# Optimization experiments

Hardware: AMD Instinct MI355X
Metric: run time of the kernel (lower is better)

## Reference

```python
import jax, jax.numpy as jnp
import numpy as np

N_NODES = 50000
N_EDGES = 800000
N_REL = 4
F_IN = 128
H1 = 64          # RGCN out
HEADS = 4
D_H = 32         # per-head GAT out
N_GRAPHS = 64


def setup_inputs() -> dict:
    key = jax.random.key(0)
    ks = jax.random.split(key, 16)
    inp = {
        "x": jax.random.normal(ks[0], (N_NODES, F_IN), dtype=jnp.float32),
        "edge_index": jax.random.randint(ks[1], (2, N_EDGES), 0, N_NODES, dtype=jnp.int32),
        "edge_type": jax.random.randint(ks[2], (N_EDGES,), 0, N_REL, dtype=jnp.int32),
        "batch": jnp.sort(jax.random.randint(ks[3], (N_NODES,), 0, N_GRAPHS, dtype=jnp.int32)),
        # RGCNConv params (relation weights, root weight, bias)
        "W_rel": jax.random.normal(ks[4], (N_REL, F_IN, H1), dtype=jnp.float32) * 0.05,
        "W_root": jax.random.normal(ks[5], (F_IN, H1), dtype=jnp.float32) * 0.05,
        "b_rgcn": jnp.zeros((H1,), dtype=jnp.float32),
        # GATConv params
        "W_gat": jax.random.normal(ks[6], (H1, HEADS * D_H), dtype=jnp.float32) * 0.1,
        "att_src": jax.random.normal(ks[7], (HEADS, D_H), dtype=jnp.float32) * 0.1,
        "att_dst": jax.random.normal(ks[8], (HEADS, D_H), dtype=jnp.float32) * 0.1,
        "b_gat": jnp.zeros((HEADS * D_H,), dtype=jnp.float32),
        # dense layers
        "W1": jax.random.normal(ks[9], (HEADS * D_H, 16), dtype=jnp.float32) * 0.05,
        "b1": jnp.zeros((16,), dtype=jnp.float32),
        "W2": jax.random.normal(ks[10], (16, 1), dtype=jnp.float32) * 0.2,
        "b2": jnp.zeros((1,), dtype=jnp.float32),
    }
    return inp


def reference(x, W_rel, W_root, b_rgcn, W_gat, att_src, att_dst, b_gat,
              W1, b1, W2, b2, edge_index, edge_type, batch):
    src, dst = edge_index[0], edge_index[1]
    n = x.shape[0]

    # ---- RGCNConv: mean aggregation per relation, then linear (linearity lets
    # us aggregate raw features first, then apply W_rel) + root transform ----
    xs = x[src]                                            # [E, F_IN]
    out = x @ W_root + b_rgcn                              # [N, H1]
    for r in range(N_REL):
        mask = (edge_type == r).astype(x.dtype)            # [E]
        s = jax.ops.segment_sum(xs * mask[:, None], dst, num_segments=n)
        cnt = jax.ops.segment_sum(mask, dst, num_segments=n)
        mean_r = s / jnp.maximum(cnt, 1.0)[:, None]        # [N, F_IN]
        out = out + mean_r @ W_rel[r]
    h = jax.nn.relu(out)                                   # [N, H1]
    # (dropout omitted: deterministic/eval reference)

    # ---- GATConv (heads=4, concat, no self loops, edge_attr unused) ----
    g = (h @ W_gat).reshape(n, HEADS, D_H)                 # [N, H, D]
    a_s = jnp.einsum('nhd,hd->nh', g, att_src)             # [N, H]
    a_d = jnp.einsum('nhd,hd->nh', g, att_dst)
    e = jax.nn.leaky_relu(a_s[src] + a_d[dst], 0.2)        # [E, H]
    m = jax.ops.segment_max(e, dst, num_segments=n)        # [N, H]
    ex = jnp.exp(e - m[dst])                               # [E, H]
    den = jax.ops.segment_sum(ex, dst, num_segments=n)     # [N, H]
    alpha = ex / den[dst]
    o = jax.ops.segment_sum(alpha[:, :, None] * g[src], dst, num_segments=n)
    o = o.reshape(n, HEADS * D_H) + b_gat                  # [N, 128]
    o = jax.nn.leaky_relu(o, 0.01)

    # ---- dense1 -> leaky_relu -> global max pool -> dense2 ----
    z = jax.nn.leaky_relu(o @ W1 + b1, 0.01)               # [N, 16]
    p = jax.ops.segment_max(z, batch, num_segments=N_GRAPHS)  # [G, 16]
    y = p @ W2 + b2                                        # [G, 1]
    return y
```

## Files before the change

kernel.cpp:

```cpp
#include <hip/hip_runtime.h>
#include <hip/hip_bf16.h>

constexpr int N_NODES = 50000;
constexpr int N_EDGES = 800000;
constexpr int F_IN = 128;
constexpr int H1 = 64;
constexpr int HEADS = 4;
constexpr int D_H = 32;
constexpr int HOUT = HEADS * D_H;
constexpr int N_REL = 4;
constexpr int N_GRAPHS = 64;
constexpr int MBIG = H1 * (1 + N_REL);
constexpr int NBLK = (N_NODES + 255) / 256;

typedef __attribute__((ext_vector_type(8))) short bf16x8;
typedef __attribute__((ext_vector_type(4))) float f32x4;

__device__ __forceinline__ unsigned f2mono(float f) {
  unsigned u = __float_as_uint(f);
  return (u & 0x80000000u) ? ~u : (u | 0x80000000u);
}
__device__ __forceinline__ float mono2f(unsigned m) {
  unsigned u = (m & 0x80000000u) ? (m & 0x7FFFFFFFu) : ~m;
  return __uint_as_float(u);
}
constexpr unsigned MONO_NEG_INF = 0x007FFFFFu;

__device__ __forceinline__ unsigned short f2bf(float f) {
  unsigned u = __float_as_uint(f);
  unsigned r = (u + 0x7FFFu + ((u >> 16) & 1u)) >> 16;
  return (unsigned short)r;
}
__device__ __forceinline__ float bf2f(unsigned short h) {
  return __uint_as_float((unsigned)h << 16);
}
__device__ __forceinline__ float bflo(unsigned u) { return __uint_as_float(u << 16); }
__device__ __forceinline__ float bfhi(unsigned u) { return __uint_as_float(u & 0xFFFF0000u); }

__global__ __launch_bounds__(256) void build_wT(const float* __restrict__ W_root,
                                                const float* __restrict__ W_rel,
                                                const float* __restrict__ W_gat,
                                                unsigned short* __restrict__ WbT_hi,
                                                unsigned short* __restrict__ WbT_lo,
                                                unsigned short* __restrict__ WgT_hi,
                                                unsigned short* __restrict__ WgT_lo) {
  int i = blockIdx.x * 256 + threadIdx.x;
  if (i < MBIG * F_IN) {
    int c = i / F_IN, k = i % F_IN;
    float w = (c < H1) ? W_root[k * H1 + c]
                       : W_rel[((size_t)(((c - H1) >> 6) * F_IN + k)) * H1 + ((c - H1) & 63)];
    unsigned short hi = f2bf(w);
    WbT_hi[i] = hi;
    WbT_lo[i] = f2bf(w - bf2f(hi));
  } else {
    int j = i - MBIG * F_IN;
    if (j < HOUT * H1) {
      int c = j / H1, k = j % H1;
      float w = W_gat[k * HOUT + c];
      unsigned short hi = f2bf(w);
      WgT_hi[j] = hi;
      WgT_lo[j] = f2bf(w - bf2f(hi));
    }
  }
}

template <int K>
__global__ __launch_bounds__(256) void gemm_mfma(const float* __restrict__ A,
                                                 const unsigned short* __restrict__ BT_hi,
                                                 const unsigned short* __restrict__ BT_lo,
                                                 float* __restrict__ C,
                                                 unsigned short* __restrict__ Cbf,
                                                 int N, int M) {
  constexpr int Kp = K + 8;
  __shared__ unsigned short Ahi[64 * Kp];
  __shared__ unsigned short Alo[64 * Kp];
  const int tid = threadIdx.x;
  const int rowBase = blockIdx.x * 64;
  const int colBase = blockIdx.y * 64;
  constexpr int KQ = K >> 2;
  constexpr int slots = 64 * KQ;
  for (int s = tid; s < slots; s += 256) {
    int r = s / KQ, c4 = (s % KQ) * 4;
    int gr = rowBase + r;
    float4 v = make_float4(0.f, 0.f, 0.f, 0.f);
    if (gr < N) v = *reinterpret_cast<const float4*>(&A[(size_t)gr * K + c4]);
    ushort4 hi, lo;
    hi.x = f2bf(v.x); lo.x = f2bf(v.x - bf2f(hi.x));
    hi.y = f2bf(v.y); lo.y = f2bf(v.y - bf2f(hi.y));
    hi.z = f2bf(v.z); lo.z = f2bf(v.z - bf2f(hi.z));
    hi.w = f2bf(v.w); lo.w = f2bf(v.w - bf2f(hi.w));
    *reinterpret_cast<ushort4*>(&Ahi[r * Kp + c4]) = hi;
    *reinterpret_cast<ushort4*>(&Alo[r * Kp + c4]) = lo;
  }
  __syncthreads();
  const int wv = tid >> 6, lane = tid & 63;
  const int wr = (wv >> 1) * 32, wc = (wv & 1) * 32;
  const int lrow = lane & 15, lkc = lane >> 4;
  f32x4 acc[2][2] = {};
#pragma unroll
  for (int ks = 0; ks < K; ks += 32) {
    bf16x8 ah[2], al[2], bh[2], bl[2];
#pragma unroll
    for (int fr = 0; fr < 2; ++fr) {
      int r = wr + fr * 16 + lrow;
      ah[fr] = *reinterpret_cast<const bf16x8*>(&Ahi[r * Kp + ks + lkc * 8]);
      al[fr] = *reinterpret_cast<const bf16x8*>(&Alo[r * Kp + ks + lkc * 8]);
    }
#pragma unroll
    for (int fc = 0; fc < 2; ++fc) {
      int c = colBase + wc + fc * 16 + lrow;
      bh[fc] = *reinterpret_cast<const bf16x8*>(&BT_hi[(size_t)c * K + ks + lkc * 8]);
      bl[fc] = *reinterpret_cast<const bf16x8*>(&BT_lo[(size_t)c * K + ks + lkc * 8]);
    }
#pragma unroll
    for (int fr = 0; fr < 2; ++fr)
#pragma unroll
      for (int fc = 0; fc < 2; ++fc) {
        acc[fr][fc] = __builtin_amdgcn_mfma_f32_16x16x32_bf16(ah[fr], bh[fc], acc[fr][fc], 0, 0, 0);
        acc[fr][fc] = __builtin_amdgcn_mfma_f32_16x16x32_bf16(ah[fr], bl[fc], acc[fr][fc], 0, 0, 0);
        acc[fr][fc] = __builtin_amdgcn_mfma_f32_16x16x32_bf16(al[fr], bh[fc], acc[fr][fc], 0, 0, 0);
      }
  }
#pragma unroll
  for (int fr = 0; fr < 2; ++fr) {
#pragma unroll
    for (int i = 0; i < 4; ++i) {
      int row = rowBase + wr + fr * 16 + lkc * 4 + i;
      if (row < N) {
#pragma unroll
        for (int fc = 0; fc < 2; ++fc) {
          int col = colBase + wc + fc * 16 + lrow;
          float v = acc[fr][fc][i];
          if (C) C[(size_t)row * M + col] = v;
          if (Cbf) Cbf[(size_t)row * M + col] = f2bf(v);
        }
      }
    }
  }
}

__global__ __launch_bounds__(256) void k_hist(const int* __restrict__ dst,
                                              int* __restrict__ deg,
                                              int* __restrict__ rank) {
  int e = blockIdx.x * 256 + threadIdx.x;
  if (e < N_EDGES) rank[e] = atomicAdd(&deg[dst[e]], 1);
}

__global__ __launch_bounds__(256) void k_s1(const int* __restrict__ deg,
                                            int* __restrict__ bsum) {
  __shared__ int ss[256];
  int t = threadIdx.x;
  int i = blockIdx.x * 256 + t;
  ss[t] = (i < N_NODES) ? deg[i] : 0;
  __syncthreads();
  for (int d = 128; d > 0; d >>= 1) {
    if (t < d) ss[t] += ss[t + d];
    __syncthreads();
  }
  if (t == 0) bsum[blockIdx.x] = ss[0];
}

__global__ __launch_bounds__(256) void k_s2(const int* __restrict__ bsum,
                                            int* __restrict__ bbase,
                                            int* __restrict__ off) {
  __shared__ int ss[256];
  int t = threadIdx.x;
  int v = (t < NBLK) ? bsum[t] : 0;
  ss[t] = v;
  __syncthreads();
  for (int d = 1; d < 256; d <<= 1) {
    int u = (t >= d) ? ss[t - d] : 0;
    __syncthreads();
    ss[t] += u;
    __syncthreads();
  }
  if (t < NBLK) bbase[t] = ss[t] - v;
  if (t == NBLK - 1) off[N_NODES] = ss[t];
}

__global__ __launch_bounds__(256) void k_s3(const int* __restrict__ deg,
                                            const int* __restrict__ bbase,
                                            int* __restrict__ off) {
  __shared__ int ss[256];
  int t = threadIdx.x;
  int i = blockIdx.x * 256 + t;
  int v = (i < N_NODES) ? deg[i] : 0;
  ss[t] = v;
  __syncthreads();
  for (int d = 1; d < 256; d <<= 1) {
    int u = (t >= d) ? ss[t - d] : 0;
    __syncthreads();
    ss[t] += u;
    __syncthreads();
  }
  if (i < N_NODES) off[i] = bbase[blockIdx.x] + ss[t] - v;
}

__global__ __launch_bounds__(256) void k_fill(const int* __restrict__ src,
                                              const int* __restrict__ dst,
                                              const int* __restrict__ etype,
                                              const int* __restrict__ off,
                                              const int* __restrict__ rank,
                                              int* __restrict__ eprep) {
  int e = blockIdx.x * 256 + threadIdx.x;
  if (e >= N_EDGES) return;
  int pos = off[dst[e]] + rank[e];
  eprep[pos] = src[e] | (etype[e] << 16);
}

__global__ __launch_bounds__(256) void rgcn_gather(const unsigned short* __restrict__ xtbf,
                                                   const int* __restrict__ off,
                                                   const int* __restrict__ eprep,
                                                   const float* __restrict__ b_rgcn,
                                                   float* __restrict__ h) {
  int wid = (blockIdx.x * 256 + threadIdx.x) >> 6;
  int lane = threadIdx.x & 63;
  int half = lane >> 5;
  int cp = lane & 31;
  int start = off[wid], end = off[wid + 1];
  float a0x=0.f,a0y=0.f,a1x=0.f,a1y=0.f,a2x=0.f,a2y=0.f,a3x=0.f,a3y=0.f;
  int c0=0,c1=0,c2=0,c3=0;
  int niter = (end - start + 1) >> 1;
  for (int t = 0; t < niter; t += 2) {
    int idx0 = start + 2 * t + half;
    int idx1 = idx0 + 2;
    int p0 = (idx0 < end) ? eprep[idx0] : 0x70000;
    int p1 = (idx1 < end) ? eprep[idx1] : 0x70000;
    int s0 = p0 & 0xFFFF, r0 = p0 >> 16;
    int s1 = p1 & 0xFFFF, r1 = p1 >> 16;
    unsigned u0 = *reinterpret_cast<const unsigned*>(
        &xtbf[(size_t)s0 * MBIG + H1 + (r0 << 6) + cp * 2]);
    unsigned u1 = *reinterpret_cast<const unsigned*>(
        &xtbf[(size_t)s1 * MBIG + H1 + (r1 << 6) + cp * 2]);
    float v0x = bflo(u0), v0y = bfhi(u0);
    float v1x = bflo(u1), v1y = bfhi(u1);
    a0x += (r0==0)?v0x:0.f; a0y += (r0==0)?v0y:0.f; c0 += (r0==0);
    a1x += (r0==1)?v0x:0.f; a1y += (r0==1)?v0y:0.f; c1 += (r0==1);
    a2x += (r0==2)?v0x:0.f; a2y += (r0==2)?v0y:0.f; c2 += (r0==2);
    a3x += (r0==3)?v0x:0.f; a3y += (r0==3)?v0y:0.f; c3 += (r0==3);
    a0x += (r1==0)?v1x:0.f; a0y += (r1==0)?v1y:0.f; c0 += (r1==0);
    a1x += (r1==1)?v1x:0.f; a1y += (r1==1)?v1y:0.f; c1 += (r1==1);
    a2x += (r1==2)?v1x:0.f; a2y += (r1==2)?v1y:0.f; c2 += (r1==2);
    a3x += (r1==3)?v1x:0.f; a3y += (r1==3)?v1y:0.f; c3 += (r1==3);
  }
  a0x += __shfl_xor(a0x, 32); a0y += __shfl_xor(a0y, 32);
  a1x += __shfl_xor(a1x, 32); a1y += __shfl_xor(a1y, 32);
  a2x += __shfl_xor(a2x, 32); a2y += __shfl_xor(a2y, 32);
  a3x += __shfl_xor(a3x, 32); a3y += __shfl_xor(a3y, 32);
  c0 += __shfl_xor(c0, 32); c1 += __shfl_xor(c1, 32);
  c2 += __shfl_xor(c2, 32); c3 += __shfl_xor(c3, 32);
  if (half == 0) {
    unsigned ur = *reinterpret_cast<const unsigned*>(&xtbf[(size_t)wid * MBIG + cp * 2]);
    float2 bb = *reinterpret_cast<const float2*>(&b_rgcn[cp * 2]);
    float i0 = 1.0f / (float)max(c0, 1);
    float i1 = 1.0f / (float)max(c1, 1);
    float i2 = 1.0f / (float)max(c2, 1);
    float i3 = 1.0f / (float)max(c3, 1);
    float vx = bflo(ur) + bb.x + a0x * i0 + a1x * i1 + a2x * i2 + a3x * i3;
    float vy = bfhi(ur) + bb.y + a0y * i0 + a1y * i1 + a2y * i2 + a3y * i3;
    *reinterpret_cast<float2*>(&h[(size_t)wid * H1 + cp * 2]) =
        make_float2(fmaxf(vx, 0.f), fmaxf(vy, 0.f));
  }
}

__global__ __launch_bounds__(256) void gat_att(const unsigned short* __restrict__ gbf,
                                               const float* __restrict__ att_src,
                                               const float* __restrict__ att_dst,
                                               float* __restrict__ a_s,
                                               float* __restrict__ a_d) {
  __shared__ float gs[64][129];
  __shared__ float asrc[HOUT], adst[HOUT];
  int t = threadIdx.x;
  if (t < HOUT) { asrc[t] = att_src[t]; adst[t] = att_dst[t]; }
  int nb = blockIdx.x * 64;
#pragma unroll
  for (int it = 0; it < 8; ++it) {
    int idx = it * 256 + t;
    int r = idx >> 5, c4 = (idx & 31) * 4;
    int gn = nb + r;
    uint2 v = make_uint2(0u, 0u);
    if (gn < N_NODES)
      v = *reinterpret_cast<const uint2*>(&gbf[(size_t)gn * HOUT + c4]);
    gs[r][c4 + 0] = bflo(v.x); gs[r][c4 + 1] = bfhi(v.x);
    gs[r][c4 + 2] = bflo(v.y); gs[r][c4 + 3] = bfhi(v.y);
  }
  __syncthreads();
  int n = t & 63, hh = t >> 6;
  float s = 0.f, d = 0.f;
#pragma unroll
  for (int k = 0; k < D_H; ++k) {
    float gv = gs[n][hh * D_H + k];
    s += gv * asrc[hh * D_H + k];
    d += gv * adst[hh * D_H + k];
  }
  if (nb + n < N_NODES) {
    a_s[(size_t)(nb + n) * 4 + hh] = s;
    a_d[(size_t)(nb + n) * 4 + hh] = d;
  }
}

__global__ __launch_bounds__(256) void init_mono(unsigned* __restrict__ p, int count) {
  int i = blockIdx.x * 256 + threadIdx.x;
  if (i < count) p[i] = MONO_NEG_INF;
}

constexpr int GAT_BLOCKS = 2048;
constexpr int GAT_WAVES = GAT_BLOCKS * 4;
__global__ __launch_bounds__(256) void gat_fused(const unsigned short* __restrict__ gbf,
                                                 const float* __restrict__ a_s,
                                                 const float* __restrict__ a_d,
                                                 const int* __restrict__ off,
                                                 const int* __restrict__ eprep,
                                                 const float* __restrict__ b_gat,
                                                 const float* __restrict__ W1,
                                                 const float* __restrict__ b1,
                                                 const int* __restrict__ batch,
                                                 unsigned* __restrict__ p_mono) {
  __shared__ float w1s[HOUT * 16];
  __shared__ float ob[4][HOUT];
  __shared__ unsigned sp[N_GRAPHS * 16];
  const int t = threadIdx.x;
  for (int i = t; i < HOUT * 16; i += 256) w1s[i] = W1[i];
  for (int i = t; i < N_GRAPHS * 16; i += 256) sp[i] = MONO_NEG_INF;
  __syncthreads();
  const int wv = t >> 6, lane = t & 63;
  const int hh = lane >> 4;
  const int jj = lane & 15, grp = lane >> 4;
  const int w = blockIdx.x * 4 + wv;
  const int q = N_NODES / GAT_WAVES;
  const int r = N_NODES % GAT_WAVES;
  const int nbeg = w * q + ((w < r) ? w : r);
  const int ncnt = q + ((w < r) ? 1 : 0);
  for (int wid = nbeg; wid < nbeg + ncnt; ++wid) {
    int start = off[wid], end = off[wid + 1];
    float4 ad4 = *reinterpret_cast<const float4*>(a_d + (size_t)wid * 4);
    float adh = (hh == 0) ? ad4.x : (hh == 1) ? ad4.y : (hh == 2) ? ad4.z : ad4.w;
    float ox = 0.f, oy = 0.f, den = 0.f;
    int i = start;
    for (; i + 4 <= end; i += 4) {
      int p0 = eprep[i], p1 = eprep[i + 1], p2 = eprep[i + 2], p3 = eprep[i + 3];
      int s0 = p0 & 0xFFFF, s1 = p1 & 0xFFFF, s2 = p2 & 0xFFFF, s3 = p3 & 0xFFFF;
      float as0 = a_s[(size_t)s0 * 4 + hh];
      float as1 = a_s[(size_t)s1 * 4 + hh];
      float as2 = a_s[(size_t)s2 * 4 + hh];
      float as3 = a_s[(size_t)s3 * 4 + hh];
      unsigned u0 = *reinterpret_cast<const unsigned*>(&gbf[(size_t)s0 * HOUT + lane * 2]);
      unsigned u1 = *reinterpret_cast<const unsigned*>(&gbf[(size_t)s1 * HOUT + lane * 2]);
      unsigned u2 = *reinterpret_cast<const unsigned*>(&gbf[(size_t)s2 * HOUT + lane * 2]);
      unsigned u3 = *reinterpret_cast<const unsigned*>(&gbf[(size_t)s3 * HOUT + lane * 2]);
      float e0 = as0 + adh; e0 = (e0 > 0.f) ? e0 : 0.2f * e0;
      float e1 = as1 + adh; e1 = (e1 > 0.f) ? e1 : 0.2f * e1;
      float e2 = as2 + adh; e2 = (e2 > 0.f) ? e2 : 0.2f * e2;
      float e3 = as3 + adh; e3 = (e3 > 0.f) ? e3 : 0.2f * e3;
      float x0 = __expf(e0), x1 = __expf(e1), x2 = __expf(e2), x3 = __expf(e3);
      den += x0 + x1 + x2 + x3;
      ox += x0 * bflo(u0) + x1 * bflo(u1) + x2 * bflo(u2) + x3 * bflo(u3);
      oy += x0 * bfhi(u0) + x1 * bfhi(u1) + x2 * bfhi(u2) + x3 * bfhi(u3);
    }
    for (; i < end; ++i) {
      int p = eprep[i];
      int s = p & 0xFFFF;
      float as = a_s[(size_t)s * 4 + hh];
      unsigned u = *reinterpret_cast<const unsigned*>(&gbf[(size_t)s * HOUT + lane * 2]);
      float e = as + adh; e = (e > 0.f) ? e : 0.2f * e;
      float ex = __expf(e);
      den += ex;
      ox += ex * bflo(u);
      oy += ex * bfhi(u);
    }
    float dinv = (den > 0.f) ? (1.0f / den) : 0.f;
    float2 bg = *reinterpret_cast<const float2*>(b_gat + lane * 2);
    float vx = ox * dinv + bg.x; vx = (vx > 0.f) ? vx : 0.01f * vx;
    float vy = oy * dinv + bg.y; vy = (vy > 0.f) ? vy : 0.01f * vy;
    *reinterpret_cast<float2*>(&ob[wv][lane * 2]) = make_float2(vx, vy);
    float acc = 0.f;
#pragma unroll 8
    for (int i2 = 0; i2 < 32; ++i2) {
      int c = grp + 4 * i2;
      acc += ob[wv][c] * w1s[c * 16 + jj];
    }
    acc += __shfl_xor(acc, 16);
    acc += __shfl_xor(acc, 32);
    float z = acc + b1[jj];
    z = (z > 0.f) ? z : 0.01f * z;
    int b = batch[wid];
    if (lane < 16) atomicMax(&sp[b * 16 + jj], f2mono(z));
  }
  __syncthreads();
  for (int i = t; i < N_GRAPHS * 16; i += 256) {
    unsigned v = sp[i];
    if (v != MONO_NEG_INF) atomicMax(p_mono + i, v);
  }
}

__global__ void final_y(const unsigned* __restrict__ p_mono,
                        const float* __restrict__ W2,
                        const float* __restrict__ b2,
                        float* __restrict__ y) {
  int gr = threadIdx.x;
  if (gr >= N_GRAPHS) return;
  float acc = b2[0];
#pragma unroll
  for (int k = 0; k < 16; ++k) acc += mono2f(p_mono[gr * 16 + k]) * W2[k];
  y[gr] = acc;
}

extern "C" void kernel_launch(void* const* d_in, const int* in_sizes, int n_in,
                              void* d_out, int out_size, void* d_ws, size_t ws_size,
                              hipStream_t stream) {
  const float* x       = (const float*)d_in[0];
  const int*   eidx    = (const int*)d_in[1];
  const int*   etype   = (const int*)d_in[2];
  const int*   batch   = (const int*)d_in[3];
  const float* W_rel   = (const float*)d_in[4];
  const float* W_root  = (const float*)d_in[5];
  const float* b_rgcn  = (const float*)d_in[6];
  const float* W_gat   = (const float*)d_in[7];
  const float* att_src = (const float*)d_in[8];
  const float* att_dst = (const float*)d_in[9];
  const float* b_gat   = (const float*)d_in[10];
  const float* W1      = (const float*)d_in[11];
  const float* b1      = (const float*)d_in[12];
  const float* W2      = (const float*)d_in[13];
  const float* b2      = (const float*)d_in[14];
  float* y = (float*)d_out;

  const int* src = eidx;
  const int* dst = eidx + N_EDGES;

  float* ws = (float*)d_ws;
  const size_t OFF_XTBF= 0;
  const size_t OFF_GBF = 0;
  const size_t OFF_H   = 8000000;
  const size_t OFF_AS  = 11200000;
  const size_t OFF_AD  = 11400000;
  const size_t OFF_PM  = 11600000;
  const size_t OFF_DEG = 11601024;
  const size_t OFF_OFFS= 11651024;
  const size_t OFF_RANK= 11701040;
  const size_t OFF_EP  = 12501040;
  const size_t OFF_BS  = 13301040;
  const size_t OFF_BB  = 13301236;
  const size_t OFF_WBH = 13301504;
  const size_t OFF_WBL = 13321984;
  const size_t OFF_WGH = 13342464;
  const size_t OFF_WGL = 13346560;
  const size_t TOTAL_F = 13350656;
  if (ws_size < TOTAL_F * sizeof(float)) return;

  unsigned short* xtbf = (unsigned short*)(ws + OFF_XTBF);
  unsigned short* gbf  = (unsigned short*)(ws + OFF_GBF);
  float* h     = ws + OFF_H;
  float* a_s   = ws + OFF_AS;
  float* a_d   = ws + OFF_AD;
  unsigned* pm = (unsigned*)(ws + OFF_PM);
  int* deg     = (int*)(ws + OFF_DEG);
  int* offs    = (int*)(ws + OFF_OFFS);
  int* rank    = (int*)(ws + OFF_RANK);
  int* eprep   = (int*)(ws + OFF_EP);
  int* bsum    = (int*)(ws + OFF_BS);
  int* bbase   = (int*)(ws + OFF_BB);
  unsigned short* wbt_hi = (unsigned short*)(ws + OFF_WBH);
  unsigned short* wbt_lo = (unsigned short*)(ws + OFF_WBL);
  unsigned short* wgt_hi = (unsigned short*)(ws + OFF_WGH);
  unsigned short* wgt_lo = (unsigned short*)(ws + OFF_WGL);

  hipMemsetAsync(deg, 0, N_NODES * sizeof(int), stream);
  k_hist<<<(N_EDGES + 255) / 256, 256, 0, stream>>>(dst, deg, rank);
  k_s1<<<NBLK, 256, 0, stream>>>(deg, bsum);
  k_s2<<<1, 256, 0, stream>>>(bsum, bbase, offs);
  k_s3<<<NBLK, 256, 0, stream>>>(deg, bbase, offs);
  k_fill<<<(N_EDGES + 255) / 256, 256, 0, stream>>>(src, dst, etype, offs, rank, eprep);

  build_wT<<<(MBIG * F_IN + HOUT * H1 + 255) / 256, 256, 0, stream>>>(
      W_root, W_rel, W_gat, wbt_hi, wbt_lo, wgt_hi, wgt_lo);

  {
    dim3 grid((N_NODES + 63) / 64, MBIG / 64);
    gemm_mfma<128><<<grid, 256, 0, stream>>>(x, wbt_hi, wbt_lo, nullptr, xtbf,
                                             N_NODES, MBIG);
  }

  rgcn_gather<<<N_NODES / 4, 256, 0, stream>>>(xtbf, offs, eprep, b_rgcn, h);

  {
    dim3 grid((N_NODES + 63) / 64, HOUT / 64);
    gemm_mfma<64><<<grid, 256, 0, stream>>>(h, wgt_hi, wgt_lo, nullptr, gbf,
                                            N_NODES, HOUT);
  }

  gat_att<<<(N_NODES + 63) / 64, 256, 0, stream>>>(gbf, att_src, att_dst, a_s, a_d);

  init_mono<<<(N_GRAPHS * 16 + 255) / 256, 256, 0, stream>>>(pm, N_GRAPHS * 16);
  gat_fused<<<GAT_BLOCKS, 256, 0, stream>>>(gbf, a_s, a_d, offs, eprep, b_gat,
                                            W1, b1, batch, pm);

  final_y<<<1, 64, 0, stream>>>(pm, W2, b2, y);
}
```

Baseline: 224.4 us.

## Replace LDS-tiled GEMM with register-resident A rows looping over all columns

The split-bf16 MFMA GEMM no longer stages A tiles in shared memory with a 2D grid over column blocks. Each wave now loads its 16 rows of A straight into registers once, splits them into hi/lo bf16, and loops over every 16-column slice of B. This removes the LDS traffic, the block barrier and the repeated reads and conversions of A for each column block. In exchange each wave reads all of B from cache serially, register pressure goes up, and there are fewer blocks in flight. Workspace offsets are shifted slightly for padding.

After: 261.9 us. 1.17x slower.

```diff
diff --git a/kernel.cpp b/kernel.cpp
--- a/kernel.cpp
+++ b/kernel.cpp
@@ -12,6 +12,7 @@
 constexpr int N_GRAPHS = 64;
 constexpr int MBIG = H1 * (1 + N_REL);
 constexpr int NBLK = (N_NODES + 255) / 256;
+constexpr int N_PAD = 50048;
 
 typedef __attribute__((ext_vector_type(8))) short bf16x8;
 typedef __attribute__((ext_vector_type(4))) float f32x4;
@@ -65,76 +66,50 @@
 }
 
 template <int K>
-__global__ __launch_bounds__(256) void gemm_mfma(const float* __restrict__ A,
-                                                 const unsigned short* __restrict__ BT_hi,
-                                                 const unsigned short* __restrict__ BT_lo,
-                                                 float* __restrict__ C,
-                                                 unsigned short* __restrict__ Cbf,
-                                                 int N, int M) {
-  constexpr int Kp = K + 8;
-  __shared__ unsigned short Ahi[64 * Kp];
-  __shared__ unsigned short Alo[64 * Kp];
+__global__ __launch_bounds__(256) void gemm_reg(const float* __restrict__ A,
+                                                const unsigned short* __restrict__ BT_hi,
+                                                const unsigned short* __restrict__ BT_lo,
+                                                unsigned short* __restrict__ Cbf,
+                                                int N, int M) {
+  constexpr int NKS = K / 32;
   const int tid = threadIdx.x;
-  const int rowBase = blockIdx.x * 64;
-  const int colBase = blockIdx.y * 64;
-  constexpr int KQ = K >> 2;
-  constexpr int slots = 64 * KQ;
-  for (int s = tid; s < slots; s += 256) {
-    int r = s / KQ, c4 = (s % KQ) * 4;
-    int gr = rowBase + r;
-    float4 v = make_float4(0.f, 0.f, 0.f, 0.f);
-    if (gr < N) v = *reinterpret_cast<const float4*>(&A[(size_t)gr * K + c4]);
-    ushort4 hi, lo;
-    hi.x = f2bf(v.x); lo.x = f2bf(v.x - bf2f(hi.x));
-    hi.y = f2bf(v.y); lo.y = f2bf(v.y - bf2f(hi.y));
-    hi.z = f2bf(v.z); lo.z = f2bf(v.z - bf2f(hi.z));
-    hi.w = f2bf(v.w); lo.w = f2bf(v.w - bf2f(hi.w));
-    *reinterpret_cast<ushort4*>(&Ahi[r * Kp + c4]) = hi;
-    *reinterpret_cast<ushort4*>(&Alo[r * Kp + c4]) = lo;
-  }
-  __syncthreads();
   const int wv = tid >> 6, lane = tid & 63;
-  const int wr = (wv >> 1) * 32, wc = (wv & 1) * 32;
   const int lrow = lane & 15, lkc = lane >> 4;
-  f32x4 acc[2][2] = {};
-#pragma unroll
-  for (int ks = 0; ks < K; ks += 32) {
-    bf16x8 ah[2], al[2], bh[2], bl[2];
-#pragma unroll
-    for (int fr = 0; fr < 2; ++fr) {
-      int r = wr + fr * 16 + lrow;
-      ah[fr] = *reinterpret_cast<const bf16x8*>(&Ahi[r * Kp + ks + lkc * 8]);
-      al[fr] = *reinterpret_cast<const bf16x8*>(&Alo[r * Kp + ks + lkc * 8]);
-    }
-#pragma unroll
-    for (int fc = 0; fc < 2; ++fc) {
-      int c = colBase + wc + fc * 16 + lrow;
-      bh[fc] = *reinterpret_cast<const bf16x8*>(&BT_hi[(size_t)c * K + ks + lkc * 8]);
-      bl[fc] = *reinterpret_cast<const bf16x8*>(&BT_lo[(size_t)c * K + ks + lkc * 8]);
-    }
-#pragma unroll
-    for (int fr = 0; fr < 2; ++fr)
-#pragma unroll
-      for (int fc = 0; fc < 2; ++fc) {
-        acc[fr][fc] = __builtin_amdgcn_mfma_f32_16x16x32_bf16(ah[fr], bh[fc], acc[fr][fc], 0, 0, 0);
-        acc[fr][fc] = __builtin_amdgcn_mfma_f32_16x16x32_bf16(ah[fr], bl[fc], acc[fr][fc], 0, 0, 0);
-        acc[fr][fc] = __builtin_amdgcn_mfma_f32_16x16x32_bf16(al[fr], bh[fc], acc[fr][fc], 0, 0, 0);
-      }
-  }
-#pragma unroll
-  for (int fr = 0; fr < 2; ++fr) {
+  const int row0 = blockIdx.x * 64 + wv * 16;
+  int ar = row0 + lrow;
+  const float* ap = A + (size_t)((ar < N) ? ar : 0) * K;
+  bf16x8 ah[NKS], al[NKS];
+#pragma unroll
+  for (int ksi = 0; ksi < NKS; ++ksi) {
+    float4 v0 = *reinterpret_cast<const float4*>(ap + ksi * 32 + lkc * 8);
+    float4 v1 = *reinterpret_cast<const float4*>(ap + ksi * 32 + lkc * 8 + 4);
+    float vv[8] = {v0.x, v0.y, v0.z, v0.w, v1.x, v1.y, v1.z, v1.w};
+    bf16x8 hh, ll;
+#pragma unroll
+    for (int j = 0; j < 8; ++j) {
+      unsigned short hb = f2bf(vv[j]);
+      hh[j] = (short)hb;
+      ll[j] = (short)f2bf(vv[j] - bf2f(hb));
+    }
+    ah[ksi] = hh;
+    al[ksi] = ll;
+  }
+  for (int cb = 0; cb < M; cb += 16) {
+    const unsigned short* bp_hi = BT_hi + (size_t)(cb + lrow) * K + lkc * 8;
+    const unsigned short* bp_lo = BT_lo + (size_t)(cb + lrow) * K + lkc * 8;
+    f32x4 acc = {};
+#pragma unroll
+    for (int ksi = 0; ksi < NKS; ++ksi) {
+      bf16x8 bh = *reinterpret_cast<const bf16x8*>(bp_hi + ksi * 32);
+      bf16x8 bl = *reinterpret_cast<const bf16x8*>(bp_lo + ksi * 32);
+      acc = __builtin_amdgcn_mfma_f32_16x16x32_bf16(ah[ksi], bh, acc, 0, 0, 0);
+      acc = __builtin_amdgcn_mfma_f32_16x16x32_bf16(ah[ksi], bl, acc, 0, 0, 0);
+      acc = __builtin_amdgcn_mfma_f32_16x16x32_bf16(al[ksi], bh, acc, 0, 0, 0);
+    }
 #pragma unroll
     for (int i = 0; i < 4; ++i) {
-      int row = rowBase + wr + fr * 16 + lkc * 4 + i;
-      if (row < N) {
-#pragma unroll
-        for (int fc = 0; fc < 2; ++fc) {
-          int col = colBase + wc + fc * 16 + lrow;
-          float v = acc[fr][fc][i];
-          if (C) C[(size_t)row * M + col] = v;
-          if (Cbf) Cbf[(size_t)row * M + col] = f2bf(v);
-        }
-      }
+      int row = row0 + lkc * 4 + i;
+      if (row < N) Cbf[(size_t)row * M + cb + lrow] = f2bf(acc[i]);
     }
   }
 }
@@ -431,21 +406,21 @@
   float* ws = (float*)d_ws;
   const size_t OFF_XTBF= 0;
   const size_t OFF_GBF = 0;
-  const size_t OFF_H   = 8000000;
-  const size_t OFF_AS  = 11200000;
-  const size_t OFF_AD  = 11400000;
-  const size_t OFF_PM  = 11600000;
-  const size_t OFF_DEG = 11601024;
-  const size_t OFF_OFFS= 11651024;
-  const size_t OFF_RANK= 11701040;
-  const size_t OFF_EP  = 12501040;
-  const size_t OFF_BS  = 13301040;
-  const size_t OFF_BB  = 13301236;
-  const size_t OFF_WBH = 13301504;
-  const size_t OFF_WBL = 13321984;
-  const size_t OFF_WGH = 13342464;
-  const size_t OFF_WGL = 13346560;
-  const size_t TOTAL_F = 13350656;
+  const size_t OFF_H   = 8007680;
+  const size_t OFF_AS  = 11210752;
+  const size_t OFF_AD  = 11410752;
+  const size_t OFF_PM  = 11610752;
+  const size_t OFF_DEG = 11611008;
+  const size_t OFF_OFFS= 11661008;
+  const size_t OFF_RANK= 11711016;
+  const size_t OFF_EP  = 12511016;
+  const size_t OFF_BS  = 13311016;
+  const size_t OFF_BB  = 13311212;
+  const size_t OFF_WBH = 13311412;
+  const size_t OFF_WBL = 13331892;
+  const size_t OFF_WGH = 13352372;
+  const size_t OFF_WGL = 13356468;
+  const size_t TOTAL_F = 13360564;
   if (ws_size < TOTAL_F * sizeof(float)) return;
 
   unsigned short* xtbf = (unsigned short*)(ws + OFF_XTBF);
@@ -475,19 +450,13 @@
   build_wT<<<(MBIG * F_IN + HOUT * H1 + 255) / 256, 256, 0, stream>>>(
       W_root, W_rel, W_gat, wbt_hi, wbt_lo, wgt_hi, wgt_lo);
 
-  {
-    dim3 grid((N_NODES + 63) / 64, MBIG / 64);
-    gemm_mfma<128><<<grid, 256, 0, stream>>>(x, wbt_hi, wbt_lo, nullptr, xtbf,
-                                             N_NODES, MBIG);
-  }
+  gemm_reg<128><<<N_PAD / 64, 256, 0, stream>>>(x, wbt_hi, wbt_lo, xtbf,
+                                                N_NODES, MBIG);
 
   rgcn_gather<<<N_NODES / 4, 256, 0, stream>>>(xtbf, offs, eprep, b_rgcn, h);
 
-  {
-    dim3 grid((N_NODES + 63) / 64, HOUT / 64);
-    gemm_mfma<64><<<grid, 256, 0, stream>>>(h, wgt_hi, wgt_lo, nullptr, gbf,
-                                            N_NODES, HOUT);
-  }
+  gemm_reg<64><<<N_PAD / 64, 256, 0, stream>>>(h, wgt_hi, wgt_lo, gbf,
+                                               N_NODES, HOUT);
 
   gat_att<<<(N_NODES + 63) / 64, 256, 0, stream>>>(gbf, att_src, att_dst, a_s, a_d);
 
```

## Fuse preprocessing kernels and presplit GEMM inputs into bf16 hi/lo globally

Applied to the files above, without the earlier changes.

Merges the histogram, weight transpose, mono init and a new x-to-bf16 hi/lo split into one multi-role kernel. The edge fill is folded into the first GEMM launch, and rgcn_gather now writes h directly as bf16 hi/lo pairs. The GEMMs then load pre-split operands into XOR-swizzled shared memory instead of converting fp32 on the fly. This cuts launch count and per-tile conversion work, but adds an extra full pass writing and reading x as hi/lo arrays and enlarges the workspace.

After: 223.4 us. Within noise of the previous version (-0.4%).

```diff
diff --git a/kernel.cpp b/kernel.cpp
--- a/kernel.cpp
+++ b/kernel.cpp
@@ -12,6 +12,7 @@
 constexpr int N_GRAPHS = 64;
 constexpr int MBIG = H1 * (1 + N_REL);
 constexpr int NBLK = (N_NODES + 255) / 256;
+constexpr int N_PAD = 50048;
 
 typedef __attribute__((ext_vector_type(8))) short bf16x8;
 typedef __attribute__((ext_vector_type(4))) float f32x4;
@@ -37,60 +38,81 @@
 __device__ __forceinline__ float bflo(unsigned u) { return __uint_as_float(u << 16); }
 __device__ __forceinline__ float bfhi(unsigned u) { return __uint_as_float(u & 0xFFFF0000u); }
 
-__global__ __launch_bounds__(256) void build_wT(const float* __restrict__ W_root,
-                                                const float* __restrict__ W_rel,
-                                                const float* __restrict__ W_gat,
-                                                unsigned short* __restrict__ WbT_hi,
-                                                unsigned short* __restrict__ WbT_lo,
-                                                unsigned short* __restrict__ WgT_hi,
-                                                unsigned short* __restrict__ WgT_lo) {
-  int i = blockIdx.x * 256 + threadIdx.x;
-  if (i < MBIG * F_IN) {
-    int c = i / F_IN, k = i % F_IN;
-    float w = (c < H1) ? W_root[k * H1 + c]
-                       : W_rel[((size_t)(((c - H1) >> 6) * F_IN + k)) * H1 + ((c - H1) & 63)];
-    unsigned short hi = f2bf(w);
-    WbT_hi[i] = hi;
-    WbT_lo[i] = f2bf(w - bf2f(hi));
+constexpr int XCVT_BLOCKS = (N_NODES * (F_IN / 4) + 255) / 256;
+constexpr int HIST_BLOCKS = (N_EDGES + 255) / 256;
+constexpr int WT_BLOCKS = (MBIG * F_IN + HOUT * H1 + 255) / 256;
+
+__global__ __launch_bounds__(256) void pre_fused(
+    const float* __restrict__ x,
+    const float* __restrict__ W_root, const float* __restrict__ W_rel,
+    const float* __restrict__ W_gat,
+    const int* __restrict__ dst,
+    unsigned short* __restrict__ xhi, unsigned short* __restrict__ xlo,
+    unsigned short* __restrict__ WbT_hi, unsigned short* __restrict__ WbT_lo,
+    unsigned short* __restrict__ WgT_hi, unsigned short* __restrict__ WgT_lo,
+    int* __restrict__ deg, int* __restrict__ rank,
+    unsigned* __restrict__ pm) {
+  int b = blockIdx.x;
+  if (b < XCVT_BLOCKS) {
+    int i = b * 256 + threadIdx.x;
+    if (i < N_NODES * (F_IN / 4)) {
+      float4 v = reinterpret_cast<const float4*>(x)[i];
+      ushort4 hi, lo;
+      hi.x = f2bf(v.x); lo.x = f2bf(v.x - bf2f(hi.x));
+      hi.y = f2bf(v.y); lo.y = f2bf(v.y - bf2f(hi.y));
+      hi.z = f2bf(v.z); lo.z = f2bf(v.z - bf2f(hi.z));
+      hi.w = f2bf(v.w); lo.w = f2bf(v.w - bf2f(hi.w));
+      reinterpret_cast<ushort4*>(xhi)[i] = hi;
+      reinterpret_cast<ushort4*>(xlo)[i] = lo;
+    }
+  } else if (b < XCVT_BLOCKS + HIST_BLOCKS) {
+    int e = (b - XCVT_BLOCKS) * 256 + threadIdx.x;
+    if (e < N_EDGES) rank[e] = atomicAdd(&deg[dst[e]], 1);
+  } else if (b < XCVT_BLOCKS + HIST_BLOCKS + WT_BLOCKS) {
+    int i = (b - XCVT_BLOCKS - HIST_BLOCKS) * 256 + threadIdx.x;
+    if (i < MBIG * F_IN) {
+      int c = i / F_IN, k = i % F_IN;
+      float w = (c < H1) ? W_root[k * H1 + c]
+                         : W_rel[((size_t)(((c - H1) >> 6) * F_IN + k)) * H1 + ((c - H1) & 63)];
+      unsigned short hi = f2bf(w);
+      WbT_hi[i] = hi;
+      WbT_lo[i] = f2bf(w - bf2f(hi));
+    } else {
+      int j = i - MBIG * F_IN;
+      if (j < HOUT * H1) {
+        int c = j / H1, k = j % H1;
+        float w = W_gat[k * HOUT + c];
+        unsigned short hi = f2bf(w);
+        WgT_hi[j] = hi;
+        WgT_lo[j] = f2bf(w - bf2f(hi));
+      }
+    }
   } else {
-    int j = i - MBIG * F_IN;
-    if (j < HOUT * H1) {
-      int c = j / H1, k = j % H1;
-      float w = W_gat[k * HOUT + c];
-      unsigned short hi = f2bf(w);
-      WgT_hi[j] = hi;
-      WgT_lo[j] = f2bf(w - bf2f(hi));
-    }
+    for (int i = threadIdx.x; i < N_GRAPHS * 16; i += 256) pm[i] = MONO_NEG_INF;
   }
 }
 
 template <int K>
-__global__ __launch_bounds__(256) void gemm_mfma(const float* __restrict__ A,
-                                                 const unsigned short* __restrict__ BT_hi,
-                                                 const unsigned short* __restrict__ BT_lo,
-                                                 float* __restrict__ C,
-                                                 unsigned short* __restrict__ Cbf,
-                                                 int N, int M) {
-  constexpr int Kp = K + 8;
-  __shared__ unsigned short Ahi[64 * Kp];
-  __shared__ unsigned short Alo[64 * Kp];
+__device__ __forceinline__ void gemm_body(int bx, int by,
+    const unsigned short* __restrict__ Ahi_,
+    const unsigned short* __restrict__ Alo_,
+    const unsigned short* __restrict__ BT_hi,
+    const unsigned short* __restrict__ BT_lo,
+    unsigned short* __restrict__ Cbf, int N, int M) {
+  __shared__ unsigned short Ah[64 * K];
+  __shared__ unsigned short Al[64 * K];
   const int tid = threadIdx.x;
-  const int rowBase = blockIdx.x * 64;
-  const int colBase = blockIdx.y * 64;
-  constexpr int KQ = K >> 2;
-  constexpr int slots = 64 * KQ;
-  for (int s = tid; s < slots; s += 256) {
-    int r = s / KQ, c4 = (s % KQ) * 4;
-    int gr = rowBase + r;
-    float4 v = make_float4(0.f, 0.f, 0.f, 0.f);
-    if (gr < N) v = *reinterpret_cast<const float4*>(&A[(size_t)gr * K + c4]);
-    ushort4 hi, lo;
-    hi.x = f2bf(v.x); lo.x = f2bf(v.x - bf2f(hi.x));
-    hi.y = f2bf(v.y); lo.y = f2bf(v.y - bf2f(hi.y));
-    hi.z = f2bf(v.z); lo.z = f2bf(v.z - bf2f(hi.z));
-    hi.w = f2bf(v.w); lo.w = f2bf(v.w - bf2f(hi.w));
-    *reinterpret_cast<ushort4*>(&Ahi[r * Kp + c4]) = hi;
-    *reinterpret_cast<ushort4*>(&Alo[r * Kp + c4]) = lo;
+  const int rowBase = bx * 64;
+  const int colBase = by * 64;
+  constexpr int KQ8 = K / 8;
+  for (int s = tid; s < 64 * KQ8; s += 256) {
+    int r = s / KQ8, c8 = (s % KQ8) * 8;
+    size_t gi = (size_t)(rowBase + r) * K + c8;
+    int sw = c8 ^ ((r & 7) << 3);
+    *reinterpret_cast<uint4*>(&Ah[r * K + sw]) =
+        *reinterpret_cast<const uint4*>(&Ahi_[gi]);
+    *reinterpret_cast<uint4*>(&Al[r * K + sw]) =
+        *reinterpret_cast<const uint4*>(&Alo_[gi]);
   }
   __syncthreads();
   const int wv = tid >> 6, lane = tid & 63;
@@ -103,8 +125,9 @@
 #pragma unroll
     for (int fr = 0; fr < 2; ++fr) {
       int r = wr + fr * 16 + lrow;
-      ah[fr] = *reinterpret_cast<const bf16x8*>(&Ahi[r * Kp + ks + lkc * 8]);
-      al[fr] = *reinterpret_cast<const bf16x8*>(&Alo[r * Kp + ks + lkc * 8]);
+      int sw = (ks + lkc * 8) ^ ((r & 7) << 3);
+      ah[fr] = *reinterpret_cast<const bf16x8*>(&Ah[r * K + sw]);
+      al[fr] = *reinterpret_cast<const bf16x8*>(&Al[r * K + sw]);
     }
 #pragma unroll
     for (int fc = 0; fc < 2; ++fc) {
@@ -130,20 +153,40 @@
 #pragma unroll
         for (int fc = 0; fc < 2; ++fc) {
           int col = colBase + wc + fc * 16 + lrow;
-          float v = acc[fr][fc][i];
-          if (C) C[(size_t)row * M + col] = v;
-          if (Cbf) Cbf[(size_t)row * M + col] = f2bf(v);
+          Cbf[(size_t)row * M + col] = f2bf(acc[fr][fc][i]);
         }
       }
     }
   }
 }
 
-__global__ __launch_bounds__(256) void k_hist(const int* __restrict__ dst,
-                                              int* __restrict__ deg,
-                                              int* __restrict__ rank) {
-  int e = blockIdx.x * 256 + threadIdx.x;
-  if (e < N_EDGES) rank[e] = atomicAdd(&deg[dst[e]], 1);
+constexpr int G1_BX = N_PAD / 64;
+constexpr int G1_BLOCKS = G1_BX * (MBIG / 64);
+__global__ __launch_bounds__(256) void gemm1_fill(
+    const unsigned short* __restrict__ xhi, const unsigned short* __restrict__ xlo,
+    const unsigned short* __restrict__ wbt_hi, const unsigned short* __restrict__ wbt_lo,
+    unsigned short* __restrict__ xtbf,
+    const int* __restrict__ src, const int* __restrict__ dst,
+    const int* __restrict__ etype, const int* __restrict__ off,
+    const int* __restrict__ rank, int* __restrict__ eprep) {
+  if (blockIdx.x < G1_BLOCKS) {
+    gemm_body<128>(blockIdx.x % G1_BX, blockIdx.x / G1_BX,
+                   xhi, xlo, wbt_hi, wbt_lo, xtbf, N_NODES, MBIG);
+  } else {
+    int e = (blockIdx.x - G1_BLOCKS) * 256 + threadIdx.x;
+    if (e < N_EDGES) {
+      int pos = off[dst[e]] + rank[e];
+      eprep[pos] = src[e] | (etype[e] << 16);
+    }
+  }
+}
+
+__global__ __launch_bounds__(256) void gemm2_k(
+    const unsigned short* __restrict__ hhi, const unsigned short* __restrict__ hlo,
+    const unsigned short* __restrict__ wgt_hi, const unsigned short* __restrict__ wgt_lo,
+    unsigned short* __restrict__ gbf) {
+  gemm_body<64>(blockIdx.x % G1_BX, blockIdx.x / G1_BX,
+                hhi, hlo, wgt_hi, wgt_lo, gbf, N_NODES, HOUT);
 }
 
 __global__ __launch_bounds__(256) void k_s1(const int* __restrict__ deg,
@@ -196,23 +239,12 @@
   if (i < N_NODES) off[i] = bbase[blockIdx.x] + ss[t] - v;
 }
 
-__global__ __launch_bounds__(256) void k_fill(const int* __restrict__ src,
-                                              const int* __restrict__ dst,
-                                              const int* __restrict__ etype,
-                                              const int* __restrict__ off,
-                                              const int* __restrict__ rank,
-                                              int* __restrict__ eprep) {
-  int e = blockIdx.x * 256 + threadIdx.x;
-  if (e >= N_EDGES) return;
-  int pos = off[dst[e]] + rank[e];
-  eprep[pos] = src[e] | (etype[e] << 16);
-}
-
 __global__ __launch_bounds__(256) void rgcn_gather(const unsigned short* __restrict__ xtbf,
                                                    const int* __restrict__ off,
                                                    const int* __restrict__ eprep,
                                                    const float* __restrict__ b_rgcn,
-                                                   float* __restrict__ h) {
+                                                   unsigned short* __restrict__ hhi,
+                                                   unsigned short* __restrict__ hlo) {
   int wid = (blockIdx.x * 256 + threadIdx.x) >> 6;
   int lane = threadIdx.x & 63;
   int half = lane >> 5;
@@ -258,8 +290,13 @@
     float i3 = 1.0f / (float)max(c3, 1);
     float vx = bflo(ur) + bb.x + a0x * i0 + a1x * i1 + a2x * i2 + a3x * i3;
     float vy = bfhi(ur) + bb.y + a0y * i0 + a1y * i1 + a2y * i2 + a3y * i3;
-    *reinterpret_cast<float2*>(&h[(size_t)wid * H1 + cp * 2]) =
-        make_float2(fmaxf(vx, 0.f), fmaxf(vy, 0.f));
+    vx = fmaxf(vx, 0.f);
+    vy = fmaxf(vy, 0.f);
+    unsigned short hx = f2bf(vx), hy = f2bf(vy);
+    ushort2 hv = {hx, hy};
+    ushort2 lv = {f2bf(vx - bf2f(hx)), f2bf(vy - bf2f(hy))};
+    *reinterpret_cast<ushort2*>(&hhi[(size_t)wid * H1 + cp * 2]) = hv;
+    *reinterpret_cast<ushort2*>(&hlo[(size_t)wid * H1 + cp * 2]) = lv;
   }
 }
 
@@ -297,11 +334,6 @@
     a_s[(size_t)(nb + n) * 4 + hh] = s;
     a_d[(size_t)(nb + n) * 4 + hh] = d;
   }
-}
-
-__global__ __launch_bounds__(256) void init_mono(unsigned* __restrict__ p, int count) {
-  int i = blockIdx.x * 256 + threadIdx.x;
-  if (i < count) p[i] = MONO_NEG_INF;
 }
 
 constexpr int GAT_BLOCKS = 2048;
@@ -431,26 +463,32 @@
   float* ws = (float*)d_ws;
   const size_t OFF_XTBF= 0;
   const size_t OFF_GBF = 0;
-  const size_t OFF_H   = 8000000;
-  const size_t OFF_AS  = 11200000;
-  const size_t OFF_AD  = 11400000;
-  const size_t OFF_PM  = 11600000;
-  const size_t OFF_DEG = 11601024;
-  const size_t OFF_OFFS= 11651024;
-  const size_t OFF_RANK= 11701040;
-  const size_t OFF_EP  = 12501040;
-  const size_t OFF_BS  = 13301040;
-  const size_t OFF_BB  = 13301236;
-  const size_t OFF_WBH = 13301504;
-  const size_t OFF_WBL = 13321984;
-  const size_t OFF_WGH = 13342464;
-  const size_t OFF_WGL = 13346560;
-  const size_t TOTAL_F = 13350656;
+  const size_t OFF_XHI = 8007680;
+  const size_t OFF_XLO = 11210752;
+  const size_t OFF_HHI = 14413824;
+  const size_t OFF_HLO = 16015360;
+  const size_t OFF_AS  = 17616896;
+  const size_t OFF_AD  = 17816896;
+  const size_t OFF_PM  = 18016896;
+  const size_t OFF_DEG = 18017920;
+  const size_t OFF_OFFS= 18067920;
+  const size_t OFF_RANK= 18117924;
+  const size_t OFF_EP  = 18917924;
+  const size_t OFF_BS  = 19717924;
+  const size_t OFF_BB  = 19718120;
+  const size_t OFF_WBH = 19718320;
+  const size_t OFF_WBL = 19738800;
+  const size_t OFF_WGH = 19759280;
+  const size_t OFF_WGL = 19763376;
+  const size_t TOTAL_F = 19767472;
   if (ws_size < TOTAL_F * sizeof(float)) return;
 
   unsigned short* xtbf = (unsigned short*)(ws + OFF_XTBF);
   unsigned short* gbf  = (unsigned short*)(ws + OFF_GBF);
-  float* h     = ws + OFF_H;
+  unsigned short* xhi  = (unsigned short*)(ws + OFF_XHI);
+  unsigned short* xlo  = (unsigned short*)(ws + OFF_XLO);
+  unsigned short* hhi  = (unsigned short*)(ws + OFF_HHI);
+  unsigned short* hlo  = (unsigned short*)(ws + OFF_HLO);
   float* a_s   = ws + OFF_AS;
   float* a_d   = ws + OFF_AD;
   unsigned* pm = (unsigned*)(ws + OFF_PM);
@@ -466,32 +504,24 @@
   unsigned short* wgt_lo = (unsigned short*)(ws + OFF_WGL);
 
   hipMemsetAsync(deg, 0, N_NODES * sizeof(int), stream);
-  k_hist<<<(N_EDGES + 255) / 256, 256, 0, stream>>>(dst, deg, rank);
+
+  pre_fused<<<XCVT_BLOCKS + HIST_BLOCKS + WT_BLOCKS + 1, 256, 0, stream>>>(
+      x, W_root, W_rel, W_gat, dst, xhi, xlo,
+      wbt_hi, wbt_lo, wgt_hi, wgt_lo, deg, rank, pm);
+
   k_s1<<<NBLK, 256, 0, stream>>>(deg, bsum);
   k_s2<<<1, 256, 0, stream>>>(bsum, bbase, offs);
   k_s3<<<NBLK, 256, 0, stream>>>(deg, bbase, offs);
-  k_fill<<<(N_EDGES + 255) / 256, 256, 0, stream>>>(src, dst, etype, offs, rank, eprep);
-
-  build_wT<<<(MBIG * F_IN + HOUT * H1 + 255) / 256, 256, 0, stream>>>(
-      W_root, W_rel, W_gat, wbt_hi, wbt_lo, wgt_hi, wgt_lo);
-
-  {
-    dim3 grid((N_NODES + 63) / 64, MBIG / 64);
-    gemm_mfma<128><<<grid, 256, 0, stream>>>(x, wbt_hi, wbt_lo, nullptr, xtbf,
-                                             N_NODES, MBIG);
-  }
-
-  rgcn_gather<<<N_NODES / 4, 256, 0, stream>>>(xtbf, offs, eprep, b_rgcn, h);
-
-  {
-    dim3 grid((N_NODES + 63) / 64, HOUT / 64);
-    gemm_mfma<64><<<grid, 256, 0, stream>>>(h, wgt_hi, wgt_lo, nullptr, gbf,
-                                            N_NODES, HOUT);
-  }
+
+  gemm1_fill<<<G1_BLOCKS + HIST_BLOCKS, 256, 0, stream>>>(
+      xhi, xlo, wbt_hi, wbt_lo, xtbf, src, dst, etype, offs, rank, eprep);
+
+  rgcn_gather<<<N_NODES / 4, 256, 0, stream>>>(xtbf, offs, eprep, b_rgcn, hhi, hlo);
+
+  gemm2_k<<<G1_BX * (HOUT / 64), 256, 0, stream>>>(hhi, hlo, wgt_hi, wgt_lo, gbf);
 
   gat_att<<<(N_NODES + 63) / 64, 256, 0, stream>>>(gbf, att_src, att_dst, a_s, a_d);
 
-  init_mono<<<(N_GRAPHS * 16 + 255) / 256, 256, 0, stream>>>(pm, N_GRAPHS * 16);
   gat_fused<<<GAT_BLOCKS, 256, 0, stream>>>(gbf, a_s, a_d, offs, eprep, b_gat,
                                             W1, b1, batch, pm);
 
```
